# Performance work log

Hardware: AMD Instinct MI355X
Metric: run time of the kernel (lower is better)

## Reference

```python
import jax, jax.numpy as jnp
import numpy as np

VOCAB = 10000
EMBED = 512
HIDDEN = 1024
FEAT = 2048
PAD_IDX = 0


def setup_inputs() -> dict:
    key = jax.random.key(0)
    ks = jax.random.split(key, 12)
    s = lambda fan_in: 1.0 / np.sqrt(fan_in)
    features = jax.random.normal(ks[0], (64, FEAT), dtype=jnp.float32)
    captions = jax.random.randint(ks[1], (64, 32), 0, VOCAB)
    embed_table = jax.random.normal(ks[2], (VOCAB, EMBED), dtype=jnp.float32) * 0.02
    embed_table = embed_table.at[PAD_IDX].set(0.0)  # padding_idx row is zero
    W_init_h = jax.random.uniform(ks[3], (HIDDEN, FEAT), jnp.float32, -s(FEAT), s(FEAT))
    b_init_h = jnp.zeros((HIDDEN,), jnp.float32)
    W_init_c = jax.random.uniform(ks[4], (HIDDEN, FEAT), jnp.float32, -s(FEAT), s(FEAT))
    b_init_c = jnp.zeros((HIDDEN,), jnp.float32)
    W_ih = jax.random.uniform(ks[5], (4 * HIDDEN, EMBED), jnp.float32, -s(HIDDEN), s(HIDDEN))
    b_ih = jax.random.uniform(ks[6], (4 * HIDDEN,), jnp.float32, -s(HIDDEN), s(HIDDEN))
    W_hh = jax.random.uniform(ks[7], (4 * HIDDEN, HIDDEN), jnp.float32, -s(HIDDEN), s(HIDDEN))
    b_hh = jax.random.uniform(ks[8], (4 * HIDDEN,), jnp.float32, -s(HIDDEN), s(HIDDEN))
    W_fc = jax.random.uniform(ks[9], (VOCAB, HIDDEN), jnp.float32, -s(HIDDEN), s(HIDDEN))
    b_fc = jax.random.uniform(ks[10], (VOCAB,), jnp.float32, -s(HIDDEN), s(HIDDEN))
    return {
        "features": features, "captions": captions, "embed_table": embed_table,
        "W_init_h": W_init_h, "b_init_h": b_init_h, "W_init_c": W_init_c, "b_init_c": b_init_c,
        "W_ih": W_ih, "b_ih": b_ih, "W_hh": W_hh, "b_hh": b_hh,
        "W_fc": W_fc, "b_fc": b_fc,
    }


def _lstm_cell(x, h, c, W_ih, b_ih, W_hh, b_hh):
    # torch LSTMCell gate order: i, f, g, o
    gates = x @ W_ih.T + b_ih + h @ W_hh.T + b_hh  # [B, 4H]
    i, f, g, o = jnp.split(gates, 4, axis=-1)
    i = jax.nn.sigmoid(i)
    f = jax.nn.sigmoid(f)
    g = jnp.tanh(g)
    o = jax.nn.sigmoid(o)
    c = f * c + i * g
    h = o * jnp.tanh(c)
    return h, c


def reference(features, captions, embed_table, W_init_h, b_init_h, W_init_c, b_init_c,
              W_ih, b_ih, W_hh, b_hh, W_fc, b_fc):
    h0 = features @ W_init_h.T + b_init_h  # [B, H]
    c0 = features @ W_init_c.T + b_init_c  # [B, H]
    emb = embed_table[captions]            # [B, T, E]
    emb_t = jnp.swapaxes(emb, 0, 1)        # [T, B, E] for scan over time

    def step(carry, x_t):
        h, c = carry
        h, c = _lstm_cell(x_t, h, c, W_ih, b_ih, W_hh, b_hh)
        out = jax.nn.sigmoid(h @ W_fc.T + b_fc)  # [B, V]
        return (h, c), out

    _, outs = jax.lax.scan(step, (h0, c0), emb_t)
    return outs  # [T, B, V] matching torch.stack(dim=0)
```

## Files before the change

### kernel.cpp

```cpp
#include <hip/hip_runtime.h>


#define B_  64
#define T_  32
#define E_  512
#define H_  1024
#define V_  10000
#define F_  2048

typedef short short8 __attribute__((ext_vector_type(8)));
typedef float floatx4 __attribute__((ext_vector_type(4)));

__device__ __forceinline__ float bf2f(unsigned short u) {
  union { unsigned int i; float f; } c; c.i = ((unsigned int)u) << 16; return c.f;
}
__device__ __forceinline__ unsigned short f2bf(float f) {
  union { float f; unsigned int i; } c; c.f = f;
  unsigned int x = c.i;
  return (unsigned short)((x + 0x7fffu + ((x >> 16) & 1u)) >> 16);
}
__device__ __forceinline__ float sigmoidf_(float x) {
  return 1.0f / (1.0f + __expf(-x));
}
__device__ __forceinline__ void gl_lds16(const unsigned short* g, unsigned short* l) {
  __builtin_amdgcn_global_load_lds(
      (const __attribute__((address_space(1))) unsigned int*)g,
      (__attribute__((address_space(3))) unsigned int*)l, 16, 0, 0);
}
__device__ __forceinline__ int xcd_swz(int lin, int nwg) {
  if (nwg < 8) return lin;
  int q = nwg >> 3, r = nwg & 7;
  int xcd = lin & 7, pos = lin >> 3;
  return (xcd < r ? xcd * (q + 1) : r * (q + 1) + (xcd - r) * q) + pos;
}

#define C_WIH  524288
#define C_WHH  1048576
#define C_WFC  2560000
#define C_WI0  524288
#define C_WC0  524288
#define C_FEA  32768
#define C_TOT  (C_WIH + C_WHH + C_WFC + C_WI0 + C_WC0 + C_FEA)
#define NFLAGW 4096

__global__ __launch_bounds__(256) void cvt_all(
    const float* __restrict__ s0, const float* __restrict__ s1,
    const float* __restrict__ s2, const float* __restrict__ s3,
    const float* __restrict__ s4, const float* __restrict__ s5,
    unsigned short* __restrict__ d0, unsigned short* __restrict__ d1,
    unsigned short* __restrict__ d2, unsigned short* __restrict__ d3,
    unsigned short* __restrict__ d4, unsigned short* __restrict__ d5,
    unsigned int* __restrict__ flags) {
  if (blockIdx.x == 0) {
    for (int w = threadIdx.x; w < NFLAGW; w += 256) flags[w] = 0u;
  }
  int i = blockIdx.x * blockDim.x + threadIdx.x;
  int stride = gridDim.x * blockDim.x;
  for (; i < C_TOT; i += stride) {
    const float* s; unsigned short* d; int j = i;
    if (j < C_WIH)            { s = s0; d = d0; }
    else if ((j -= C_WIH) < C_WHH) { s = s1; d = d1; }
    else if ((j -= C_WHH) < C_WFC) { s = s2; d = d2; }
    else if ((j -= C_WFC) < C_WI0) { s = s3; d = d3; }
    else if ((j -= C_WI0) < C_WC0) { s = s4; d = d4; }
    else { j -= C_WC0; s = s5; d = d5; }
    float4 v = ((const float4*)s)[j];
    ushort4 o;
    o.x = f2bf(v.x); o.y = f2bf(v.y); o.z = f2bf(v.z); o.w = f2bf(v.w);
    ((ushort4*)d)[j] = o;
  }
}

__global__ __launch_bounds__(128) void embed_gather(
    const float* __restrict__ table, const int* __restrict__ captions,
    unsigned short* __restrict__ out) {
  int row = blockIdx.x;
  int t = row >> 6, b = row & 63;
  int idx = captions[b * T_ + t];
  const float4* src = (const float4*)(table + (size_t)idx * E_);
  ushort4* dst = (ushort4*)(out + (size_t)row * E_);
  for (int e = threadIdx.x; e < E_ / 4; e += blockDim.x) {
    float4 v = src[e];
    ushort4 o;
    o.x = f2bf(v.x); o.y = f2bf(v.y); o.z = f2bf(v.z); o.w = f2bf(v.w);
    dst[e] = o;
  }
}

template <int ACT_SIGMOID, int OUT_BF16, int OUT_INIT>
__global__ __launch_bounds__(256) void mfma_gemm128(
    const unsigned short* __restrict__ A, const unsigned short* __restrict__ W,
    const float* __restrict__ bias1, const float* __restrict__ bias2,
    void* __restrict__ out, void* __restrict__ out2, int M, int N, int K) {
  __shared__ unsigned short At[2][128 * 32];
  __shared__ unsigned short Wt[2][128 * 32];

  const int tid  = threadIdx.x;
  const int lane = tid & 63;
  const int wave = tid >> 6;
  const int l15  = lane & 15;
  const int quad = lane >> 4;
  const int wm   = (wave >> 1) * 64;
  const int wn   = (wave & 1) * 64;

  const int gx  = gridDim.x;
  const int nwg = gx * gridDim.y;
  const int wg  = xcd_swz(blockIdx.y * gx + blockIdx.x, nwg);
  const int m0  = (wg % gx) * 128;
  const int n0  = (wg / gx) * 128;
  const int ksl = (quad ^ (l15 & 3)) * 8;

  const int c0i = tid, c1i = tid + 256;
  const int ar0 = c0i >> 2, ak0 = (((c0i & 3) ^ (ar0 & 3)) * 8);
  const int ar1 = c1i >> 2, ak1 = (((c1i & 3) ^ (ar1 & 3)) * 8);
  int am0 = m0 + ar0; if (am0 > M - 1) am0 = M - 1;
  int am1 = m0 + ar1; if (am1 > M - 1) am1 = M - 1;
  int wn0 = n0 + ar0; if (wn0 > N - 1) wn0 = N - 1;
  int wn1 = n0 + ar1; if (wn1 > N - 1) wn1 = N - 1;
  const unsigned short* Ag0 = A + (size_t)am0 * K + ak0;
  const unsigned short* Ag1 = A + (size_t)am1 * K + ak1;
  const unsigned short* Wg0 = W + (size_t)wn0 * K + ak0;
  const unsigned short* Wg1 = W + (size_t)wn1 * K + ak1;

  floatx4 acc[4][4];
#pragma unroll
  for (int i = 0; i < 4; ++i)
#pragma unroll
    for (int j = 0; j < 4; ++j) acc[i][j] = (floatx4){0.f, 0.f, 0.f, 0.f};

  gl_lds16(Ag0, &At[0][c0i * 8]);
  gl_lds16(Ag1, &At[0][c1i * 8]);
  gl_lds16(Wg0, &Wt[0][c0i * 8]);
  gl_lds16(Wg1, &Wt[0][c1i * 8]);
  __syncthreads();

  int cur = 0;
  for (int k0 = 0; k0 < K; k0 += 32) {
    const int kn = k0 + 32;
    if (kn < K) {
      const int nb = cur ^ 1;
      gl_lds16(Ag0 + kn, &At[nb][c0i * 8]);
      gl_lds16(Ag1 + kn, &At[nb][c1i * 8]);
      gl_lds16(Wg0 + kn, &Wt[nb][c0i * 8]);
      gl_lds16(Wg1 + kn, &Wt[nb][c1i * 8]);
    }
    short8 a[4], b[4];
#pragma unroll
    for (int mt = 0; mt < 4; ++mt)
      a[mt] = *(const short8*)&At[cur][(wm + mt * 16 + l15) * 32 + ksl];
#pragma unroll
    for (int nt = 0; nt < 4; ++nt)
      b[nt] = *(const short8*)&Wt[cur][(wn + nt * 16 + l15) * 32 + ksl];
#pragma unroll
    for (int mt = 0; mt < 4; ++mt)
#pragma unroll
      for (int nt = 0; nt < 4; ++nt)
        acc[mt][nt] = __builtin_amdgcn_mfma_f32_16x16x32_bf16(a[mt], b[nt], acc[mt][nt], 0, 0, 0);
    __syncthreads();
    cur ^= 1;
  }

#pragma unroll
  for (int nt = 0; nt < 4; ++nt) {
    int col = n0 + wn + nt * 16 + l15;
    if (col >= N) continue;
    float bsum;
    if (OUT_INIT)
      bsum = (col < H_) ? bias1[col] : bias2[col - H_];
    else
      bsum = (bias1 ? bias1[col] : 0.f) + (bias2 ? bias2[col] : 0.f);
#pragma unroll
    for (int mt = 0; mt < 4; ++mt) {
#pragma unroll
      for (int r = 0; r < 4; ++r) {
        int m = m0 + wm + mt * 16 + quad * 4 + r;
        if (m >= M) continue;
        float v = acc[mt][nt][r] + bsum;
        if (ACT_SIGMOID) v = sigmoidf_(v);
        if (OUT_INIT) {
          if (col < H_)
            ((unsigned short*)out)[(size_t)m * H_ + col] = f2bf(v);
          else
            ((float*)out2)[(size_t)m * H_ + (col - H_)] = v;
        } else if (OUT_BF16) {
          ((unsigned short*)out)[(size_t)m * N + col] = f2bf(v);
        } else {
          ((float*)out)[(size_t)m * N + col] = v;
        }
      }
    }
  }
}

#define WSPAD2 1032
__global__ __launch_bounds__(512, 2) void lstm_persistent(
    const unsigned short* __restrict__ W_hh_b,
    const unsigned short* __restrict__ gx_b,
    const float* __restrict__ c0_f32,
    unsigned short* __restrict__ h_all,
    unsigned int* __restrict__ flags) {
  __shared__ unsigned short Ws[32 * WSPAD2];
  __shared__ float gbuf[4][32][33];

  const int tid  = threadIdx.x;
  const int lane = tid & 63;
  const int wave = tid >> 6;
  const int l15  = lane & 15;
  const int quad = lane >> 4;
  const int kb   = quad * 8;
  const int bid  = blockIdx.x;
  const int cg   = bid >> 1;
  const int bh   = bid & 1;
  const int colbase = cg * 8;
  const int kq   = wave >> 1;
  const int mt   = wave & 1;

#pragma unroll
  for (int it = 0; it < 8; ++it) {
    int u = wave * 8 + it;
    int n = u >> 1, half = u & 1;
    int grow = (n >> 3) * H_ + colbase + (n & 7);
    gl_lds16(W_hh_b + (size_t)grow * H_ + half * 512 + lane * 8,
             &Ws[n * WSPAD2 + half * 512]);
  }

  const int bq = tid >> 2;
  const int cp = tid & 3;
  const int gb = bh * 32 + bq;
  float cA = 0.f, cB = 0.f;
  if (tid < 128) {
    float2 cv = *(const float2*)(c0_f32 + (size_t)gb * H_ + colbase + 2 * cp);
    cA = cv.x; cB = cv.y;
  }

  const unsigned short* hbase =
      h_all + (size_t)(bh * 32 + mt * 16 + l15) * H_ + kq * 256 + kb;
  const unsigned short* wb0 = &Ws[(size_t)(l15)      * WSPAD2 + kq * 256 + kb];
  const unsigned short* wb1 = &Ws[(size_t)(16 + l15) * WSPAD2 + kq * 256 + kb];
  const unsigned int* pf0 = flags + (size_t)(2 * lane        + bh) * 16;
  const unsigned int* pf1 = flags + (size_t)(2 * (lane + 64) + bh) * 16;

  __syncthreads();

  for (int t = 0; t < T_; ++t) {
    const unsigned short* hp = hbase + (size_t)t * (B_ * H_);
    short8 hx[8];
#pragma unroll
    for (int i = 0; i < 8; ++i)
      asm volatile("global_load_dwordx4 %0, %1, off sc0 sc1"
                   : "=v"(hx[i]) : "v"(hp + i * 32) : "memory");

    unsigned int ui = 0, uf = 0, ug = 0, uo = 0;
    if (tid < 128) {
      const unsigned short* gxp =
          gx_b + (size_t)t * (B_ * 4 * H_) + (size_t)gb * (4 * H_) + colbase + 2 * cp;
      ui = *(const unsigned int*)(gxp + 0 * H_);
      uf = *(const unsigned int*)(gxp + 1 * H_);
      ug = *(const unsigned int*)(gxp + 2 * H_);
      uo = *(const unsigned int*)(gxp + 3 * H_);
    }

    asm volatile("s_waitcnt vmcnt(0)" ::: "memory");
    __builtin_amdgcn_sched_barrier(0);

    floatx4 A0 = (floatx4){0.f, 0.f, 0.f, 0.f}, A1 = A0;
#pragma unroll
    for (int i = 0; i < 8; ++i) {
      short8 w0 = *(const short8*)(wb0 + i * 32);
      short8 w1 = *(const short8*)(wb1 + i * 32);
      A0 = __builtin_amdgcn_mfma_f32_16x16x32_bf16(hx[i], w0, A0, 0, 0, 0);
      A1 = __builtin_amdgcn_mfma_f32_16x16x32_bf16(hx[i], w1, A1, 0, 0, 0);
    }
#pragma unroll
    for (int r = 0; r < 4; ++r) {
      gbuf[kq][mt * 16 + quad * 4 + r][l15]      = A0[r];
      gbuf[kq][mt * 16 + quad * 4 + r][16 + l15] = A1[r];
    }
    __syncthreads();

    if (tid < 128) {
      const int c0c = 2 * cp, c1c = 2 * cp + 1;
      float giA = gbuf[0][bq][ 0 + c0c] + gbuf[1][bq][ 0 + c0c]
                + gbuf[2][bq][ 0 + c0c] + gbuf[3][bq][ 0 + c0c] + bf2f((unsigned short)(ui & 0xffff));
      float gfA = gbuf[0][bq][ 8 + c0c] + gbuf[1][bq][ 8 + c0c]
                + gbuf[2][bq][ 8 + c0c] + gbuf[3][bq][ 8 + c0c] + bf2f((unsigned short)(uf & 0xffff));
      float ggA = gbuf[0][bq][16 + c0c] + gbuf[1][bq][16 + c0c]
                + gbuf[2][bq][16 + c0c] + gbuf[3][bq][16 + c0c] + bf2f((unsigned short)(ug & 0xffff));
      float goA = gbuf[0][bq][24 + c0c] + gbuf[1][bq][24 + c0c]
                + gbuf[2][bq][24 + c0c] + gbuf[3][bq][24 + c0c] + bf2f((unsigned short)(uo & 0xffff));
      float giB = gbuf[0][bq][ 0 + c1c] + gbuf[1][bq][ 0 + c1c]
                + gbuf[2][bq][ 0 + c1c] + gbuf[3][bq][ 0 + c1c] + bf2f((unsigned short)(ui >> 16));
      float gfB = gbuf[0][bq][ 8 + c1c] + gbuf[1][bq][ 8 + c1c]
                + gbuf[2][bq][ 8 + c1c] + gbuf[3][bq][ 8 + c1c] + bf2f((unsigned short)(uf >> 16));
      float ggB = gbuf[0][bq][16 + c1c] + gbuf[1][bq][16 + c1c]
                + gbuf[2][bq][16 + c1c] + gbuf[3][bq][16 + c1c] + bf2f((unsigned short)(ug >> 16));
      float goB = gbuf[0][bq][24 + c1c] + gbuf[1][bq][24 + c1c]
                + gbuf[2][bq][24 + c1c] + gbuf[3][bq][24 + c1c] + bf2f((unsigned short)(uo >> 16));
      giA = sigmoidf_(giA); gfA = sigmoidf_(gfA); ggA = tanhf(ggA); goA = sigmoidf_(goA);
      giB = sigmoidf_(giB); gfB = sigmoidf_(gfB); ggB = tanhf(ggB); goB = sigmoidf_(goB);
      cA = gfA * cA + giA * ggA;
      cB = gfB * cB + giB * ggB;
      float hA = goA * tanhf(cA);
      float hB = goB * tanhf(cB);
      unsigned int hv = (unsigned int)f2bf(hA) | ((unsigned int)f2bf(hB) << 16);
      unsigned int* hop = (unsigned int*)(h_all + (size_t)(t + 1) * (B_ * H_)
                                          + (size_t)gb * H_ + colbase + 2 * cp);
      asm volatile("global_store_dword %0, %1, off sc0 sc1"
                   :: "v"(hop), "v"(hv) : "memory");
      asm volatile("s_waitcnt vmcnt(0)" ::: "memory");
    }

    if (t < T_ - 1) {
      __syncthreads();
      const unsigned int tgt = (unsigned int)(t + 1);
      if (tid == 0) {
        unsigned int* myf = flags + (size_t)bid * 16;
        asm volatile("global_store_dword %0, %1, off sc0 sc1"
                     :: "v"(myf), "v"(tgt) : "memory");
      }
      if (wave == 0) {
        unsigned int a, b;
        do {
          asm volatile("global_load_dword %0, %1, off sc0 sc1"
                       : "=v"(a) : "v"(pf0) : "memory");
          asm volatile("global_load_dword %0, %1, off sc0 sc1"
                       : "=v"(b) : "v"(pf1) : "memory");
          asm volatile("s_waitcnt vmcnt(0)" ::: "memory");
        } while (!__all(a >= tgt && b >= tgt));
      }
      __syncthreads();
    }
  }
}

extern "C" void kernel_launch(void* const* d_in, const int* in_sizes, int n_in,
                              void* d_out, int out_size, void* d_ws, size_t ws_size,
                              hipStream_t stream) {
  const float* features    = (const float*)d_in[0];
  const int*   captions    = (const int*)d_in[1];
  const float* embed_table = (const float*)d_in[2];
  const float* W_init_h    = (const float*)d_in[3];
  const float* b_init_h    = (const float*)d_in[4];
  const float* W_init_c    = (const float*)d_in[5];
  const float* b_init_c    = (const float*)d_in[6];
  const float* W_ih        = (const float*)d_in[7];
  const float* b_ih        = (const float*)d_in[8];
  const float* W_hh        = (const float*)d_in[9];
  const float* b_hh        = (const float*)d_in[10];
  const float* W_fc        = (const float*)d_in[11];
  const float* b_fc        = (const float*)d_in[12];
  float* out = (float*)d_out;

  char* ws = (char*)d_ws;
  auto alloc = [&](size_t bytes) -> char* {
    char* p = ws;
    ws += (bytes + 255) & ~(size_t)255;
    return p;
  };
  unsigned short* W_ih_b  = (unsigned short*)alloc((size_t)4 * H_ * E_ * 2);
  unsigned short* W_hh_b  = (unsigned short*)alloc((size_t)4 * H_ * H_ * 2);
  unsigned short* W_fc_b  = (unsigned short*)alloc((size_t)V_ * H_ * 2);
  unsigned short* Wih0_b  = (unsigned short*)alloc((size_t)H_ * F_ * 2);
  unsigned short* Wic0_b  = (unsigned short*)alloc((size_t)H_ * F_ * 2);
  unsigned short* feat_b  = (unsigned short*)alloc((size_t)B_ * F_ * 2);
  unsigned short* emb_b   = (unsigned short*)alloc((size_t)T_ * B_ * E_ * 2);
  unsigned short* gx_b    = (unsigned short*)alloc((size_t)T_ * B_ * 4 * H_ * 2);
  unsigned short* h_all   = (unsigned short*)alloc((size_t)(T_ + 1) * B_ * H_ * 2);
  float*          c_f32   = (float*)alloc((size_t)B_ * H_ * 4);
  unsigned int*   flags   = (unsigned int*)alloc((size_t)NFLAGW * 4);
  (void)ws_size; (void)in_sizes; (void)n_in; (void)out_size; (void)Wic0_b;

  hipLaunchKernelGGL(cvt_all, dim3(4096), dim3(256), 0, stream,
                     W_ih, W_hh, W_fc, W_init_h, W_init_c, features,
                     W_ih_b, W_hh_b, W_fc_b, Wih0_b, Wic0_b, feat_b, flags);

  hipLaunchKernelGGL(embed_gather, dim3(T_ * B_), dim3(128), 0, stream,
                     embed_table, captions, emb_b);

  hipLaunchKernelGGL((mfma_gemm128<0, 1, 1>), dim3(1, 2 * H_ / 128), dim3(256), 0, stream,
                     feat_b, Wih0_b, b_init_h, b_init_c,
                     (void*)h_all, (void*)c_f32, B_, 2 * H_, F_);

  hipLaunchKernelGGL((mfma_gemm128<0, 1, 0>), dim3(T_ * B_ / 128, 4 * H_ / 128), dim3(256), 0, stream,
                     emb_b, W_ih_b, b_ih, b_hh, (void*)gx_b, (void*)nullptr,
                     T_ * B_, 4 * H_, E_);

  hipLaunchKernelGGL(lstm_persistent, dim3(2 * H_ / 8), dim3(512), 0, stream,
                     W_hh_b, gx_b, c_f32, h_all, flags);

  hipLaunchKernelGGL((mfma_gemm128<1, 0, 0>), dim3(T_ * B_ / 128, (V_ + 127) / 128), dim3(256), 0, stream,
                     h_all + (size_t)B_ * H_, W_fc_b, b_fc, (const float*)nullptr,
                     (void*)out, (void*)nullptr, T_ * B_, V_, H_);
}
```

Baseline: 483.7 us.

## Fuse output FC projection into persistent LSTM kernel, overlapping with recurrence

Removes the separate output GEMM launch and instead has waves 1-6 of each persistent LSTM block compute a 40-column slab of the vocab projection for the previous timestep while wave 0 polls the grid barrier. The barrier now waits on all 256 block flags instead of only the blocks sharing its batch half, and sleeps between polls. The aim is to hide the large FC GEMM behind the latency-bound recurrence. In exchange the FC work reads W_fc and h directly from global memory without LDS tiling, and it can lengthen each step if it runs past the barrier wait.

```diff
diff --git a/kernel.cpp b/kernel.cpp
--- a/kernel.cpp
+++ b/kernel.cpp
@@ -192,13 +192,58 @@
   }
 }
 
+__device__ __forceinline__ void fc_slab(
+    const unsigned short* __restrict__ hsrc,
+    const unsigned short* __restrict__ W_fc_b,
+    const float* __restrict__ b_fc,
+    float* __restrict__ orow,
+    int vb, int wave, int l15, int quad) {
+  const int t0 = (wave - 1) * 2, t1 = t0 + 1;
+  const int bf0 = t0 / 3, cf0 = t0 % 3;
+  const int bf1 = t1 / 3, cf1 = t1 % 3;
+  const int kq8 = quad * 8;
+  const int c0 = vb + cf0 * 16 + l15;
+  const int c1 = vb + cf1 * 16 + l15;
+  const int wr0 = c0 < V_ ? c0 : V_ - 1;
+  const int wr1 = c1 < V_ ? c1 : V_ - 1;
+  const unsigned short* a0p = hsrc + (size_t)(bf0 * 16 + l15) * H_ + kq8;
+  const unsigned short* a1p = hsrc + (size_t)(bf1 * 16 + l15) * H_ + kq8;
+  const unsigned short* b0p = W_fc_b + (size_t)wr0 * H_ + kq8;
+  const unsigned short* b1p = W_fc_b + (size_t)wr1 * H_ + kq8;
+  floatx4 acc0 = (floatx4){0.f, 0.f, 0.f, 0.f}, acc1 = acc0;
+#pragma unroll 4
+  for (int k = 0; k < H_; k += 32) {
+    short8 a0 = *(const short8*)(a0p + k);
+    short8 b0 = *(const short8*)(b0p + k);
+    short8 a1 = *(const short8*)(a1p + k);
+    short8 b1 = *(const short8*)(b1p + k);
+    acc0 = __builtin_amdgcn_mfma_f32_16x16x32_bf16(a0, b0, acc0, 0, 0, 0);
+    acc1 = __builtin_amdgcn_mfma_f32_16x16x32_bf16(a1, b1, acc1, 0, 0, 0);
+  }
+  if (c0 < vb + 40 && c0 < V_) {
+    const float bs = b_fc[c0];
+#pragma unroll
+    for (int r = 0; r < 4; ++r)
+      orow[(size_t)(bf0 * 16 + quad * 4 + r) * V_ + c0] = sigmoidf_(acc0[r] + bs);
+  }
+  if (c1 < vb + 40 && c1 < V_) {
+    const float bs = b_fc[c1];
+#pragma unroll
+    for (int r = 0; r < 4; ++r)
+      orow[(size_t)(bf1 * 16 + quad * 4 + r) * V_ + c1] = sigmoidf_(acc1[r] + bs);
+  }
+}
+
 #define WSPAD2 1032
 __global__ __launch_bounds__(512, 2) void lstm_persistent(
     const unsigned short* __restrict__ W_hh_b,
     const unsigned short* __restrict__ gx_b,
     const float* __restrict__ c0_f32,
     unsigned short* __restrict__ h_all,
-    unsigned int* __restrict__ flags) {
+    unsigned int* __restrict__ flags,
+    const unsigned short* __restrict__ W_fc_b,
+    const float* __restrict__ b_fc,
+    float* __restrict__ out) {
   __shared__ unsigned short Ws[32 * WSPAD2];
   __shared__ float gbuf[4][32][33];
 
@@ -214,6 +259,7 @@
   const int colbase = cg * 8;
   const int kq   = wave >> 1;
   const int mt   = wave & 1;
+  const int vb   = bid * 40;
 
 #pragma unroll
   for (int it = 0; it < 8; ++it) {
@@ -237,19 +283,14 @@
       h_all + (size_t)(bh * 32 + mt * 16 + l15) * H_ + kq * 256 + kb;
   const unsigned short* wb0 = &Ws[(size_t)(l15)      * WSPAD2 + kq * 256 + kb];
   const unsigned short* wb1 = &Ws[(size_t)(16 + l15) * WSPAD2 + kq * 256 + kb];
-  const unsigned int* pf0 = flags + (size_t)(2 * lane        + bh) * 16;
-  const unsigned int* pf1 = flags + (size_t)(2 * (lane + 64) + bh) * 16;
+  const unsigned int* pf0 = flags + (size_t)(lane)       * 16;
+  const unsigned int* pf1 = flags + (size_t)(lane + 64)  * 16;
+  const unsigned int* pf2 = flags + (size_t)(lane + 128) * 16;
+  const unsigned int* pf3 = flags + (size_t)(lane + 192) * 16;
 
   __syncthreads();
 
   for (int t = 0; t < T_; ++t) {
-    const unsigned short* hp = hbase + (size_t)t * (B_ * H_);
-    short8 hx[8];
-#pragma unroll
-    for (int i = 0; i < 8; ++i)
-      asm volatile("global_load_dwordx4 %0, %1, off sc0 sc1"
-                   : "=v"(hx[i]) : "v"(hp + i * 32) : "memory");
-
     unsigned int ui = 0, uf = 0, ug = 0, uo = 0;
     if (tid < 128) {
       const unsigned short* gxp =
@@ -260,6 +301,12 @@
       uo = *(const unsigned int*)(gxp + 3 * H_);
     }
 
+    const unsigned short* hp = hbase + (size_t)t * (B_ * H_);
+    short8 hx[8];
+#pragma unroll
+    for (int i = 0; i < 8; ++i)
+      asm volatile("global_load_dwordx4 %0, %1, off sc0 sc1"
+                   : "=v"(hx[i]) : "v"(hp + i * 32) : "memory");
     asm volatile("s_waitcnt vmcnt(0)" ::: "memory");
     __builtin_amdgcn_sched_barrier(0);
 
@@ -310,27 +357,57 @@
       asm volatile("s_waitcnt vmcnt(0)" ::: "memory");
     }
 
-    if (t < T_ - 1) {
-      __syncthreads();
+    __syncthreads();
+    if (tid == 0) {
+      const unsigned int tg = (unsigned int)(t + 1);
+      unsigned int* myf = flags + (size_t)bid * 16;
+      asm volatile("global_store_dword %0, %1, off sc0 sc1"
+                   :: "v"(myf), "v"(tg) : "memory");
+    }
+    if (t > 0 && wave >= 1 && wave <= 6 && vb < V_)
+      fc_slab(h_all + (size_t)t * (B_ * H_), W_fc_b, b_fc,
+              out + (size_t)(t - 1) * (B_ * V_), vb, wave, l15, quad);
+    if (t < T_ - 1 && wave == 0) {
       const unsigned int tgt = (unsigned int)(t + 1);
-      if (tid == 0) {
-        unsigned int* myf = flags + (size_t)bid * 16;
-        asm volatile("global_store_dword %0, %1, off sc0 sc1"
-                     :: "v"(myf), "v"(tgt) : "memory");
+      for (;;) {
+        unsigned int v0, v1, v2, v3;
+        asm volatile("global_load_dword %0, %1, off sc0 sc1"
+                     : "=v"(v0) : "v"(pf0) : "memory");
+        asm volatile("global_load_dword %0, %1, off sc0 sc1"
+                     : "=v"(v1) : "v"(pf1) : "memory");
+        asm volatile("global_load_dword %0, %1, off sc0 sc1"
+                     : "=v"(v2) : "v"(pf2) : "memory");
+        asm volatile("global_load_dword %0, %1, off sc0 sc1"
+                     : "=v"(v3) : "v"(pf3) : "memory");
+        asm volatile("s_waitcnt vmcnt(0)" ::: "memory");
+        if (__all(v0 >= tgt && v1 >= tgt && v2 >= tgt && v3 >= tgt)) break;
+        __builtin_amdgcn_s_sleep(1);
       }
-      if (wave == 0) {
-        unsigned int a, b;
-        do {
-          asm volatile("global_load_dword %0, %1, off sc0 sc1"
-                       : "=v"(a) : "v"(pf0) : "memory");
-          asm volatile("global_load_dword %0, %1, off sc0 sc1"
-                       : "=v"(b) : "v"(pf1) : "memory");
-          asm volatile("s_waitcnt vmcnt(0)" ::: "memory");
-        } while (!__all(a >= tgt && b >= tgt));
-      }
-      __syncthreads();
-    }
-  }
+    }
+    __syncthreads();
+  }
+
+  if (wave == 0) {
+    const unsigned int tgt = (unsigned int)T_;
+    for (;;) {
+      unsigned int v0, v1, v2, v3;
+      asm volatile("global_load_dword %0, %1, off sc0 sc1"
+                   : "=v"(v0) : "v"(pf0) : "memory");
+      asm volatile("global_load_dword %0, %1, off sc0 sc1"
+                   : "=v"(v1) : "v"(pf1) : "memory");
+      asm volatile("global_load_dword %0, %1, off sc0 sc1"
+                   : "=v"(v2) : "v"(pf2) : "memory");
+      asm volatile("global_load_dword %0, %1, off sc0 sc1"
+                   : "=v"(v3) : "v"(pf3) : "memory");
+      asm volatile("s_waitcnt vmcnt(0)" ::: "memory");
+      if (__all(v0 >= tgt && v1 >= tgt && v2 >= tgt && v3 >= tgt)) break;
+      __builtin_amdgcn_s_sleep(1);
+    }
+  }
+  __syncthreads();
+  if (wave >= 1 && wave <= 6 && vb < V_)
+    fc_slab(h_all + (size_t)T_ * (B_ * H_), W_fc_b, b_fc,
+            out + (size_t)(T_ - 1) * (B_ * V_), vb, wave, l15, quad);
 }
 
 extern "C" void kernel_launch(void* const* d_in, const int* in_sizes, int n_in,
@@ -386,9 +463,5 @@
                      T_ * B_, 4 * H_, E_);
 
   hipLaunchKernelGGL(lstm_persistent, dim3(2 * H_ / 8), dim3(512), 0, stream,
-                     W_hh_b, gx_b, c_f32, h_all, flags);
-
-  hipLaunchKernelGGL((mfma_gemm128<1, 0, 0>), dim3(T_ * B_ / 128, (V_ + 127) / 128), dim3(256), 0, stream,
-                     h_all + (size_t)B_ * H_, W_fc_b, b_fc, (const float*)nullptr,
-                     (void*)out, (void*)nullptr, T_ * B_, V_, H_);
-}
+                     W_hh_b, gx_b, c_f32, h_all, flags, W_fc_b, b_fc, out);
+}
```

Measured after the change: 1.109 ms. +129.3%, slower.
